# Kernel optimization log

Measured on AMD Instinct MI355X. Metric: run time of the kernel, lower is better.

Reference implementation:

```python
import jax, jax.numpy as jnp
import numpy as np

NEIGHB = 16   # k neighbors
GROUP = 32    # GroupNorm groups (== outc/2 -> per-channel instance norm)
EPS = 1e-5


def _lrelu(x, slope):
    return jnp.where(x >= 0, x, slope * x)


def _gn(x, gamma, beta, groups=GROUP, eps=EPS):
    # GroupNorm over [B, C, S, K]
    B, C, S, K = x.shape
    xr = x.reshape(B, groups, (C // groups) * S * K)
    m = xr.mean(-1, keepdims=True)
    v = xr.var(-1, keepdims=True)
    xn = ((xr - m) * jax.lax.rsqrt(v + eps)).reshape(B, C, S, K)
    return xn * gamma[None, :, None, None] + beta[None, :, None, None]


def _sample(x, rand_num, s_num, k):
    # Dynamic_sampling.forward, s_num <= P branch (s_num == P here)
    B, C, P = x.shape
    perm = jnp.argsort(rand_num, axis=1)[:, :s_num]                    # [B,S]
    sel = jnp.take_along_axis(x, perm[:, None, :], axis=2)             # [B,C,S]
    x3, s3 = x[:, :3], sel[:, :3]
    # pairwise = -||xi - qj||^2, shape [B,P,S]
    pd = -(jnp.sum(x3 * x3, 1)[:, :, None]
           - 2.0 * jnp.einsum('bcp,bcs->bps', x3, s3)
           + jnp.sum(s3 * s3, 1)[:, None, :])
    _, idx = jax.lax.top_k(pd.transpose(0, 2, 1), k)                   # [B,S,k]
    # torch: topk(dim=-2) gives [B,k,S], then .view(B,s_num,k) -> row-major
    # reinterpretation (NOT a transpose). Replicate exactly:
    idx = idx.transpose(0, 2, 1).reshape(B, s_num, k)
    xT = x.transpose(0, 2, 1)                                          # [B,P,C]
    feat = jax.vmap(lambda xt, ii: xt[ii])(xT, idx)                    # [B,S,k,C]
    return feat.transpose(0, 3, 1, 2)                                  # [B,C,S,k]


def _forward(x, rand_num, w_pe, g_pe, b_pe, w_conv, g_conv, b_conv,
             w_att1, w_att2, w_b1, w_b2, num_points):
    x1 = _sample(x, jax.lax.stop_gradient(rand_num), num_points, NEIGHB)  # [B,4,S,K]
    PA = x1[:, :3]                                                        # [B,3,S,K]
    PC = x1[:, :3, :, 0:1]                                                # [B,3,S,1]
    diff = PA - PC
    # safe sqrt: diff at K=0 is exactly 0 -> clamp to keep grads finite
    temp = jnp.sqrt(jnp.clip(jnp.sum(diff * diff, 1, keepdims=True), 1e-12))
    PEmb = jnp.concatenate([PA, jnp.broadcast_to(PC, PA.shape), diff, temp], axis=1)  # [B,10,S,K]
    PEmb = _lrelu(_gn(jnp.einsum('oc,bcsk->bosk', w_pe, PEmb), g_pe, b_pe), 0.2)
    x_ = _lrelu(_gn(jnp.einsum('oc,bcsk->bosk', w_conv, x1), g_conv, b_conv), 0.2)
    feature = jnp.concatenate([x_, PEmb], axis=1)                         # [B,64,S,K]
    att = jnp.einsum('oc,bcsk->bosk', w_att2,
                     _lrelu(jnp.einsum('oc,bcsk->bosk', w_att1, feature), 0.2))
    att = jax.nn.softmax(att, axis=-1)                                    # over K
    feature = jnp.sum(feature * att, axis=-1)                             # [B,64,S]
    Fea1 = jnp.einsum('oc,bcs->bos', w_b1, feature)
    Fea2 = jnp.einsum('oc,bcs->bos', w_b2, x1[:, :, :, 0])
    out = _lrelu(Fea1 + Fea2, 0.1)
    return jnp.concatenate([x1[:, :3, :, 0], out], axis=1)                # [B,67,S]


def setup_inputs() -> dict:
    key = jax.random.key(0)
    ks = jax.random.split(key, 10)
    B, C, P = 2, 4, 8192
    sc = 0.1
    x = jax.random.normal(ks[0], (B, C, P), jnp.float32)
    rand_num = jax.random.uniform(ks[1], (B, P), jnp.float32)
    w_pe = jax.random.normal(ks[2], (32, 10), jnp.float32) * sc
    g_pe = jnp.ones((32,), jnp.float32)
    b_pe = jnp.zeros((32,), jnp.float32)
    w_conv = jax.random.normal(ks[3], (32, 4), jnp.float32) * sc
    g_conv = jnp.ones((32,), jnp.float32)
    b_conv = jnp.zeros((32,), jnp.float32)
    w_att1 = jax.random.normal(ks[4], (32, 64), jnp.float32) * sc
    w_att2 = jax.random.normal(ks[5], (1, 32), jnp.float32) * sc
    w_b1 = jax.random.normal(ks[6], (64, 64), jnp.float32) * sc
    w_b2 = jax.random.normal(ks[7], (64, 4), jnp.float32) * sc
    return dict(x=x, rand_num=rand_num, w_pe=w_pe, g_pe=g_pe, b_pe=b_pe,
                w_conv=w_conv, g_conv=g_conv, b_conv=b_conv,
                w_att1=w_att1, w_att2=w_att2, w_b1=w_b1, w_b2=w_b2,
                num_points=8192)


def reference(x, rand_num, w_pe, g_pe, b_pe, w_conv, g_conv, b_conv,
              w_att1, w_att2, w_b1, w_b2, num_points):
    return _forward(x, rand_num, w_pe, g_pe, b_pe, w_conv, g_conv, b_conv,
                    w_att1, w_att2, w_b1, w_b2, num_points)
```

## Files before the change

kernel.cpp:

```cpp
#include <hip/hip_runtime.h>
#include <stdint.h>

#define PN 8192
#define SN 8192
#define KNB 16
#define SUBS 4
#define NCH1 8
#define CHUNK1 256
#define NCOL 8
#define COLCH (PN / NCOL)
#define SEGCAP 32
#define MARGIN 1.0e-3f
#define NRCH 8
#define RCH (PN / NRCH)

#define KEY_SENTINEL ((long long)0x8000000000000000ULL)
#define PD_SCALE 2199023255552.0

__device__ __forceinline__ void bitonic_sort16(float* b) {
#pragma unroll
    for (int k = 2; k <= 16; k <<= 1) {
#pragma unroll
        for (int j = k >> 1; j > 0; j >>= 1) {
#pragma unroll
            for (int i = 0; i < 16; ++i) {
                int l = i ^ j;
                if (l > i) {
                    float lo = fminf(b[i], b[l]), hi = fmaxf(b[i], b[l]);
                    bool up = ((i & k) == 0);
                    b[i] = up ? lo : hi;
                    b[l] = up ? hi : lo;
                }
            }
        }
    }
}
__device__ __forceinline__ void merge16(float* r, const float* b) {
    float t[16];
#pragma unroll
    for (int i = 0; i < 16; ++i) t[i] = fminf(r[i], b[15 - i]);
#pragma unroll
    for (int j = 8; j > 0; j >>= 1) {
#pragma unroll
        for (int i = 0; i < 16; ++i) {
            int l = i ^ j;
            if (l > i) {
                float lo = fminf(t[i], t[l]), hi = fmaxf(t[i], t[l]);
                t[i] = lo; t[l] = hi;
            }
        }
    }
#pragma unroll
    for (int i = 0; i < 16; ++i) r[i] = t[i];
}

__global__ void pack_pts_kernel(const float* __restrict__ x, float4* __restrict__ pts) {
    int i = blockIdx.x * 256 + threadIdx.x;
    int b = i >> 13, p = i & (PN - 1);
    const float* xb = x + (size_t)b * 4 * PN;
    pts[i] = make_float4(xb[p], xb[PN + p], xb[2 * PN + p], 0.f);
}

__global__ __launch_bounds__(256) void rank_count_kernel(const float* __restrict__ rnd,
        unsigned short* __restrict__ rcnt) {
    __shared__ unsigned long long lk[RCH];
    const int chunk = blockIdx.x, sg = blockIdx.y, b = blockIdx.z;
    const unsigned int* rb = (const unsigned int*)rnd + b * PN;
    const int cbase = chunk * RCH;
    for (int c = threadIdx.x; c < RCH; c += 256) {
        int j = cbase + c;
        lk[c] = ((unsigned long long)rb[j] << 13) | (unsigned)j;
    }
    __syncthreads();
    const int i = sg * 256 + threadIdx.x;
    const unsigned long long ki = ((unsigned long long)rb[i] << 13) | (unsigned)i;
    int cnt = 0;
#pragma unroll 8
    for (int c = 0; c < RCH; ++c) cnt += (lk[c] < ki) ? 1 : 0;
    rcnt[(((size_t)(b * NRCH + chunk)) << 13) + i] = (unsigned short)cnt;
}

__global__ void rank_scatter_kernel(const unsigned short* __restrict__ rcnt,
                                    int* __restrict__ perm) {
    int t = blockIdx.x * 256 + threadIdx.x;
    int b = t >> 13, i = t & (PN - 1);
    int rank = 0;
#pragma unroll
    for (int ch = 0; ch < NRCH; ++ch)
        rank += rcnt[(((size_t)(b * NRCH + ch)) << 13) + i];
    perm[b * PN + rank] = i;
}

__global__ __launch_bounds__(256) void knn_val16_kernel(const float4* __restrict__ pts,
        const int* __restrict__ perm, float* __restrict__ vv) {
    const int chunk = blockIdx.x, sg = blockIdx.y, b = blockIdx.z;
    const float4* pb = pts + b * PN;
    const int pbase = chunk * CHUNK1;
    const int s = sg * 256 + threadIdx.x;
    const float4 qp = pb[perm[b * PN + s]];
    float r[16];
#pragma unroll
    for (int i = 0; i < 16; ++i) r[i] = 3.0e38f;
    for (int t = 0; t < CHUNK1; t += 16) {
        float bv[16];
#pragma unroll
        for (int u = 0; u < 16; ++u) {
            float4 pp = pb[SUBS * (pbase + t + u)];
            float dx = qp.x - pp.x, dy = qp.y - pp.y, dz = qp.z - pp.z;
            bv[u] = dx * dx + dy * dy + dz * dz;
        }
        bitonic_sort16(bv);
        merge16(r, bv);
    }
    float* ov = vv + ((size_t)(b * NCH1 + chunk) * 16) * SN + s;
#pragma unroll
    for (int i = 0; i < 16; ++i) ov[(size_t)i * SN] = r[i];
}

__global__ void knn_thr_kernel(const float* __restrict__ vv, float* __restrict__ thrbuf) {
    int t = blockIdx.x * 256 + threadIdx.x;
    int b = t >> 13, s = t & (SN - 1);
    float r[16], bl[16];
    const float* v0 = vv + ((size_t)(b * NCH1) * 16) * SN + s;
#pragma unroll
    for (int i = 0; i < 16; ++i) r[i] = v0[(size_t)i * SN];
    for (int ch = 1; ch < NCH1; ++ch) {
        const float* vc = vv + ((size_t)(b * NCH1 + ch) * 16) * SN + s;
#pragma unroll
        for (int i = 0; i < 16; ++i) bl[i] = vc[(size_t)i * SN];
        merge16(r, bl);
    }
    thrbuf[b * SN + s] = r[15] + MARGIN;
}

#define COLPROC(pp, cidx) do { \
    float dx_ = qp.x - (pp).x, dy_ = qp.y - (pp).y, dz_ = qp.z - (pp).z; \
    float dd_ = dx_ * dx_; dd_ += dy_ * dy_; dd_ += dz_ * dz_; \
    if (dd_ < thr) { if (cnt < SEGCAP) seg[cnt] = (unsigned short)(cidx); ++cnt; } \
} while (0)

__global__ __launch_bounds__(256) void knn_collect_kernel(const float4* __restrict__ pts,
        const int* __restrict__ perm, const float* __restrict__ thrbuf,
        unsigned short* __restrict__ segcnt, unsigned short* __restrict__ segIdx) {
    const int chunk = blockIdx.x, sg = blockIdx.y, b = blockIdx.z;
    const float4* pb = pts + b * PN;
    const int pbase = chunk * COLCH;
    const int s = sg * 256 + threadIdx.x;
    const int bs = b * SN + s;
    const float4 qp = pb[perm[bs]];
    const float thr = thrbuf[bs];
    unsigned short* seg = segIdx + ((size_t)bs * NCOL + chunk) * SEGCAP;
    int cnt = 0;
    const float4* cp = pb + pbase;
    float4 a0 = cp[0], a1 = cp[1], a2 = cp[2], a3 = cp[3];
    float4 a4 = cp[4], a5 = cp[5], a6 = cp[6], a7 = cp[7];
    int c = 0;
    for (; c < COLCH - 8; c += 8) {
        float4 n0 = cp[c + 8],  n1 = cp[c + 9],  n2 = cp[c + 10], n3 = cp[c + 11];
        float4 n4 = cp[c + 12], n5 = cp[c + 13], n6 = cp[c + 14], n7 = cp[c + 15];
        COLPROC(a0, pbase + c + 0);
        COLPROC(a1, pbase + c + 1);
        COLPROC(a2, pbase + c + 2);
        COLPROC(a3, pbase + c + 3);
        COLPROC(a4, pbase + c + 4);
        COLPROC(a5, pbase + c + 5);
        COLPROC(a6, pbase + c + 6);
        COLPROC(a7, pbase + c + 7);
        a0 = n0; a1 = n1; a2 = n2; a3 = n3;
        a4 = n4; a5 = n5; a6 = n6; a7 = n7;
    }
    COLPROC(a0, pbase + c + 0);
    COLPROC(a1, pbase + c + 1);
    COLPROC(a2, pbase + c + 2);
    COLPROC(a3, pbase + c + 3);
    COLPROC(a4, pbase + c + 4);
    COLPROC(a5, pbase + c + 5);
    COLPROC(a6, pbase + c + 6);
    COLPROC(a7, pbase + c + 7);
    segcnt[(size_t)bs * NCOL + chunk] = (unsigned short)cnt;
}

#define MAKEKEY(pp, c, out) do { \
    double dx_ = qx - (double)(pp).x; \
    double dy_ = qy - (double)(pp).y; \
    double dz_ = qz - (double)(pp).z; \
    double dd_ = dx_ * dx_ + dy_ * dy_ + dz_ * dz_; \
    long long sc_ = (long long)floor(-dd_ * PD_SCALE); \
    (out) = (sc_ << 13) | (long long)(8191 - (c)); \
} while (0)

#define INS16(kkv) do { long long nk = (kkv); if (nk > k15) { \
    k15 = (nk > k14) ? k14 : ((nk > k15) ? nk : k15); \
    k14 = (nk > k13) ? k13 : ((nk > k14) ? nk : k14); \
    k13 = (nk > k12) ? k12 : ((nk > k13) ? nk : k13); \
    k12 = (nk > k11) ? k11 : ((nk > k12) ? nk : k12); \
    k11 = (nk > k10) ? k10 : ((nk > k11) ? nk : k11); \
    k10 = (nk > k9 ) ? k9  : ((nk > k10) ? nk : k10); \
    k9  = (nk > k8 ) ? k8  : ((nk > k9 ) ? nk : k9 ); \
    k8  = (nk > k7 ) ? k7  : ((nk > k8 ) ? nk : k8 ); \
    k7  = (nk > k6 ) ? k6  : ((nk > k7 ) ? nk : k7 ); \
    k6  = (nk > k5 ) ? k5  : ((nk > k6 ) ? nk : k6 ); \
    k5  = (nk > k4 ) ? k4  : ((nk > k5 ) ? nk : k5 ); \
    k4  = (nk > k3 ) ? k3  : ((nk > k4 ) ? nk : k4 ); \
    k3  = (nk > k2 ) ? k2  : ((nk > k3 ) ? nk : k3 ); \
    k2  = (nk > k1 ) ? k1  : ((nk > k2 ) ? nk : k2 ); \
    k1  = (nk > k0 ) ? k0  : ((nk > k1 ) ? nk : k1 ); \
    k0  = (nk > k0 ) ? nk  : k0; \
} } while (0)

__global__ __launch_bounds__(256) void knn_exact_kernel(const float4* __restrict__ pts,
        const int* __restrict__ perm, const unsigned short* __restrict__ segcnt,
        const unsigned short* __restrict__ segIdx, int* __restrict__ knn) {
    int t = blockIdx.x * 256 + threadIdx.x;
    int b = t >> 13, s = t & (SN - 1);
    const int bs = b * SN + s;
    const float4* pb = pts + b * PN;
    const float4 qp = pb[perm[bs]];
    const double qx = qp.x, qy = qp.y, qz = qp.z;
    long long k0 = KEY_SENTINEL, k1 = KEY_SENTINEL, k2 = KEY_SENTINEL, k3 = KEY_SENTINEL,
              k4 = KEY_SENTINEL, k5 = KEY_SENTINEL, k6 = KEY_SENTINEL, k7 = KEY_SENTINEL,
              k8 = KEY_SENTINEL, k9 = KEY_SENTINEL, k10 = KEY_SENTINEL, k11 = KEY_SENTINEL,
              k12 = KEY_SENTINEL, k13 = KEY_SENTINEL, k14 = KEY_SENTINEL, k15 = KEY_SENTINEL;
    const unsigned short* scp = segcnt + (size_t)bs * NCOL;
    ushort4 c03 = *reinterpret_cast<const ushort4*>(scp);
    ushort4 c47 = *reinterpret_cast<const ushort4*>(scp + 4);
    int ns[NCOL] = {c03.x, c03.y, c03.z, c03.w, c47.x, c47.y, c47.z, c47.w};
    bool ovf = false;
#pragma unroll
    for (int ch = 0; ch < NCOL; ++ch) ovf |= (ns[ch] > SEGCAP);
    if (!ovf) {
        const unsigned short* base = segIdx + (size_t)bs * (NCOL * SEGCAP);
#pragma unroll
        for (int ch = 0; ch < NCOL; ++ch) {
            const unsigned short* seg = base + ch * SEGCAP;
            const int n = ns[ch];
            for (int u = 0; u < n; u += 4) {
                ushort4 i4 = *reinterpret_cast<const ushort4*>(seg + u);
                int c0i = (int)i4.x;
                int c1i = (u + 1 < n) ? (int)i4.y : 0;
                int c2i = (u + 2 < n) ? (int)i4.z : 0;
                int c3i = (u + 3 < n) ? (int)i4.w : 0;
                float4 p0 = pb[c0i], p1 = pb[c1i], p2 = pb[c2i], p3 = pb[c3i];
                long long kk0, kk1, kk2, kk3;
                MAKEKEY(p0, c0i, kk0);
                MAKEKEY(p1, c1i, kk1);
                MAKEKEY(p2, c2i, kk2);
                MAKEKEY(p3, c3i, kk3);
                kk1 = (u + 1 < n) ? kk1 : KEY_SENTINEL;
                kk2 = (u + 2 < n) ? kk2 : KEY_SENTINEL;
                kk3 = (u + 3 < n) ? kk3 : KEY_SENTINEL;
                INS16(kk0);
                INS16(kk1);
                INS16(kk2);
                INS16(kk3);
            }
        }
    } else {
        for (int c = 0; c < PN; ++c) {
            float4 pp = pb[c];
            long long kk;
            MAKEKEY(pp, c, kk);
            INS16(kk);
        }
    }
    int* ob = knn + (size_t)b * (SN * KNB);
    ob[(size_t)0 * SN + s]  = 8191 - (int)(k0 & 8191);
    ob[(size_t)1 * SN + s]  = 8191 - (int)(k1 & 8191);
    ob[(size_t)2 * SN + s]  = 8191 - (int)(k2 & 8191);
    ob[(size_t)3 * SN + s]  = 8191 - (int)(k3 & 8191);
    ob[(size_t)4 * SN + s]  = 8191 - (int)(k4 & 8191);
    ob[(size_t)5 * SN + s]  = 8191 - (int)(k5 & 8191);
    ob[(size_t)6 * SN + s]  = 8191 - (int)(k6 & 8191);
    ob[(size_t)7 * SN + s]  = 8191 - (int)(k7 & 8191);
    ob[(size_t)8 * SN + s]  = 8191 - (int)(k8 & 8191);
    ob[(size_t)9 * SN + s]  = 8191 - (int)(k9 & 8191);
    ob[(size_t)10 * SN + s] = 8191 - (int)(k10 & 8191);
    ob[(size_t)11 * SN + s] = 8191 - (int)(k11 & 8191);
    ob[(size_t)12 * SN + s] = 8191 - (int)(k12 & 8191);
    ob[(size_t)13 * SN + s] = 8191 - (int)(k13 & 8191);
    ob[(size_t)14 * SN + s] = 8191 - (int)(k14 & 8191);
    ob[(size_t)15 * SN + s] = 8191 - (int)(k15 & 8191);
}

__global__ __launch_bounds__(256) void stats_kernel(const float* __restrict__ x,
        const int* __restrict__ knn, const float* __restrict__ w_pe,
        const float* __restrict__ w_conv, float* __restrict__ wavepart) {
    const int blk = blockIdx.x;
    const int b = blockIdx.y;
    const int w = threadIdx.x >> 6, l = threadIdx.x & 63;
    float wr[10];
#pragma unroll
    for (int c = 0; c < 10; ++c) wr[c] = 0.f;
    if (l < 32) {
#pragma unroll
        for (int c = 0; c < 4; ++c) wr[c] = w_conv[l * 4 + c];
    } else {
#pragma unroll
        for (int c = 0; c < 10; ++c) wr[c] = w_pe[(l - 32) * 10 + c];
    }
    const float* xb = x + (size_t)b * 4 * PN;
    const int* kb = knn + (size_t)b * (SN * KNB);
    float s1 = 0.f, s2 = 0.f;
    const int nbase = blk * 512 + w * 128;
#pragma unroll 2
    for (int it = 0; it < 128; ++it) {
        int n = nbase + it;
        int i  = kb[n];
        int i0 = kb[n & ~15];
        float xa0 = xb[i], xa1 = xb[PN + i], xa2 = xb[2 * PN + i], xa3 = xb[3 * PN + i];
        float xc0 = xb[i0], xc1 = xb[PN + i0], xc2 = xb[2 * PN + i0];
        float d0 = xa0 - xc0, d1 = xa1 - xc1, d2 = xa2 - xc2;
        float dd = d0 * d0; dd += d1 * d1; dd += d2 * d2;
        float temp = sqrtf(fmaxf(dd, 1e-12f));
        float r;
        if (l < 32) {
            r = wr[0] * xa0 + wr[1] * xa1 + wr[2] * xa2 + wr[3] * xa3;
        } else {
            r = wr[0] * xa0 + wr[1] * xa1 + wr[2] * xa2
              + wr[3] * xc0 + wr[4] * xc1 + wr[5] * xc2
              + wr[6] * d0 + wr[7] * d1 + wr[8] * d2 + wr[9] * temp;
        }
        s1 += r;
        s2 += r * r;
    }
    const int wslot = blk * 4 + w;
    wavepart[((size_t)b * 1024 + wslot) * 128 + l] = s1;
    wavepart[((size_t)b * 1024 + wslot) * 128 + 64 + l] = s2;
}

__global__ void finalize_kernel(const float* __restrict__ wavepart,
        const float* __restrict__ g_pe, const float* __restrict__ b_pe,
        const float* __restrict__ g_conv, const float* __restrict__ b_conv,
        float* __restrict__ scsh) {
    const int t = threadIdx.x;
    const int b = t >> 7, k = t & 127;
    float acc = 0.f;
    for (int w = 0; w < 1024; ++w) acc += wavepart[((size_t)b * 1024 + w) * 128 + k];
    __shared__ float sums[2][128];
    sums[b][k] = acc;
    __syncthreads();
    if (k < 64) {
        const float N = 131072.f;
        float mean = sums[b][k] / N;
        float var = sums[b][64 + k] / N - mean * mean;
        float rstd = 1.0f / sqrtf(var + 1e-5f);
        float gam = (k < 32) ? g_conv[k] : g_pe[k - 32];
        float bet = (k < 32) ? b_conv[k] : b_pe[k - 32];
        float sc = gam * rstd;
        scsh[(b * 64 + k) * 2 + 0] = sc;
        scsh[(b * 64 + k) * 2 + 1] = bet - mean * sc;
    }
}

__global__ __launch_bounds__(256) void fused_main_kernel(
        const float* __restrict__ x, const int* __restrict__ knn,
        const float* __restrict__ w_pe, const float* __restrict__ w_conv,
        const float* __restrict__ w_att1, const float* __restrict__ w_att2,
        const float* __restrict__ w_b1, const float* __restrict__ w_b2,
        const float* __restrict__ scsh, float* __restrict__ out) {
    __shared__ float wb1T[64 * 64];
    __shared__ float wb2T[4 * 64];
    for (int i = threadIdx.x; i < 64 * 64; i += 256) wb1T[(i & 63) * 64 + (i >> 6)] = w_b1[i];
    { int i = threadIdx.x; wb2T[(i & 3) * 64 + (i >> 2)] = w_b2[i]; }
    __syncthreads();
    const int gidx = blockIdx.x;
    const int b = gidx >> 9;
    const int sb = (gidx & 511) << 4;
    const int l = threadIdx.x & 63;
    const int w = threadIdx.x >> 6;
    const int g = l >> 4, j = l & 15;
    const int s = sb + (w << 2) + g;
    const int srcl = g << 4;
    const float* xb = x + (size_t)b * 4 * PN;
    const int i1 = knn[(size_t)b * (SN * KNB) + (size_t)s * KNB + j];
    float xa0 = xb[i1], xa1 = xb[PN + i1], xa2 = xb[2 * PN + i1], xa3 = xb[3 * PN + i1];
    float xc0 = __shfl(xa0, srcl), xc1 = __shfl(xa1, srcl);
    float xc2 = __shfl(xa2, srcl), xc3 = __shfl(xa3, srcl);
    float d0 = xa0 - xc0, d1 = xa1 - xc1, d2 = xa2 - xc2;
    float dd = d0 * d0; dd += d1 * d1; dd += d2 * d2;
    float temp = sqrtf(fmaxf(dd, 1e-12f));
    float pem[10] = {xa0, xa1, xa2, xc0, xc1, xc2, d0, d1, d2, temp};
    float f[64];
    const float* ssb = scsh + b * 128;
#pragma unroll
    for (int o = 0; o < 32; ++o) {
        float r = w_conv[o * 4 + 0] * xa0;
        r += w_conv[o * 4 + 1] * xa1;
        r += w_conv[o * 4 + 2] * xa2;
        r += w_conv[o * 4 + 3] * xa3;
        r = r * ssb[o * 2 + 0] + ssb[o * 2 + 1];
        f[o] = (r >= 0.f) ? r : 0.2f * r;
    }
#pragma unroll
    for (int o = 0; o < 32; ++o) {
        float r = 0.f;
#pragma unroll
        for (int c = 0; c < 10; ++c) r += w_pe[o * 10 + c] * pem[c];
        r = r * ssb[(32 + o) * 2 + 0] + ssb[(32 + o) * 2 + 1];
        f[32 + o] = (r >= 0.f) ? r : 0.2f * r;
    }
    float logit = 0.f;
#pragma unroll 2
    for (int o = 0; o < 32; ++o) {
        float a = 0.f;
#pragma unroll
        for (int c = 0; c < 64; ++c) a += w_att1[o * 64 + c] * f[c];
        a = (a >= 0.f) ? a : 0.2f * a;
        logit += w_att2[o] * a;
    }
    float mx = logit;
    mx = fmaxf(mx, __shfl_xor(mx, 1));
    mx = fmaxf(mx, __shfl_xor(mx, 2));
    mx = fmaxf(mx, __shfl_xor(mx, 4));
    mx = fmaxf(mx, __shfl_xor(mx, 8));
    float e = expf(logit - mx);
    float se = e;
    se += __shfl_xor(se, 1);
    se += __shfl_xor(se, 2);
    se += __shfl_xor(se, 4);
    se += __shfl_xor(se, 8);
    float att = e / se;
#pragma unroll
    for (int c = 0; c < 64; ++c) {
        float v = f[c] * att;
        v += __shfl_xor(v, 1);
        v += __shfl_xor(v, 2);
        v += __shfl_xor(v, 4);
        v += __shfl_xor(v, 8);
        f[c] = v;
    }
    float o0 = 0.f, o1 = 0.f, o2 = 0.f, o3 = 0.f;
#pragma unroll
    for (int c = 0; c < 64; ++c) {
        float4 wv = *reinterpret_cast<const float4*>(&wb1T[c * 64 + 4 * j]);
        o0 += wv.x * f[c]; o1 += wv.y * f[c]; o2 += wv.z * f[c]; o3 += wv.w * f[c];
    }
    {
        float4 wv = *reinterpret_cast<const float4*>(&wb2T[0 * 64 + 4 * j]);
        o0 += wv.x * xc0; o1 += wv.y * xc0; o2 += wv.z * xc0; o3 += wv.w * xc0;
        wv = *reinterpret_cast<const float4*>(&wb2T[1 * 64 + 4 * j]);
        o0 += wv.x * xc1; o1 += wv.y * xc1; o2 += wv.z * xc1; o3 += wv.w * xc1;
        wv = *reinterpret_cast<const float4*>(&wb2T[2 * 64 + 4 * j]);
        o0 += wv.x * xc2; o1 += wv.y * xc2; o2 += wv.z * xc2; o3 += wv.w * xc2;
        wv = *reinterpret_cast<const float4*>(&wb2T[3 * 64 + 4 * j]);
        o0 += wv.x * xc3; o1 += wv.y * xc3; o2 += wv.z * xc3; o3 += wv.w * xc3;
    }
    o0 = (o0 >= 0.f) ? o0 : 0.1f * o0;
    o1 = (o1 >= 0.f) ? o1 : 0.1f * o1;
    o2 = (o2 >= 0.f) ? o2 : 0.1f * o2;
    o3 = (o3 >= 0.f) ? o3 : 0.1f * o3;
    float* ob = out + (size_t)b * 67 * SN;
    const int oc = 3 + 4 * j;
    ob[(size_t)(oc + 0) * SN + s] = o0;
    ob[(size_t)(oc + 1) * SN + s] = o1;
    ob[(size_t)(oc + 2) * SN + s] = o2;
    ob[(size_t)(oc + 3) * SN + s] = o3;
    if (j < 3) ob[(size_t)j * SN + s] = (j == 0) ? xc0 : ((j == 1) ? xc1 : xc2);
}

extern "C" void kernel_launch(void* const* d_in, const int* in_sizes, int n_in,
                              void* d_out, int out_size, void* d_ws, size_t ws_size,
                              hipStream_t stream) {
    (void)in_sizes; (void)n_in; (void)out_size; (void)ws_size;
    const float* x      = (const float*)d_in[0];
    const float* rnd    = (const float*)d_in[1];
    const float* w_pe   = (const float*)d_in[2];
    const float* g_pe   = (const float*)d_in[3];
    const float* b_pe   = (const float*)d_in[4];
    const float* w_conv = (const float*)d_in[5];
    const float* g_conv = (const float*)d_in[6];
    const float* b_conv = (const float*)d_in[7];
    const float* w_att1 = (const float*)d_in[8];
    const float* w_att2 = (const float*)d_in[9];
    const float* w_b1   = (const float*)d_in[10];
    const float* w_b2   = (const float*)d_in[11];
    float* out = (float*)d_out;
    char* ws = (char*)d_ws;
    float4*         pts    = (float4*)        (ws + 0);
    int*            perm   = (int*)           (ws + 262144);
    unsigned short* rcnt   = (unsigned short*)(ws + 327680);
    float*          vv     = (float*)         (ws + 327680);
    unsigned short* segIdx = (unsigned short*)(ws + 327680);
    float*          wavept = (float*)         (ws + 327680);
    float*          thrbuf = (float*)         (ws + 8716288);
    unsigned short* segcnt = (unsigned short*)(ws + 8781824);
    int*            knn    = (int*)           (ws + 9043968);
    float*          scsh   = (float*)         (ws + 10092544);

    pack_pts_kernel<<<64, 256, 0, stream>>>(x, pts);
    rank_count_kernel<<<dim3(NRCH, 32, 2), 256, 0, stream>>>(rnd, rcnt);
    rank_scatter_kernel<<<64, 256, 0, stream>>>(rcnt, perm);
    knn_val16_kernel<<<dim3(NCH1, 32, 2), 256, 0, stream>>>(pts, perm, vv);
    knn_thr_kernel<<<64, 256, 0, stream>>>(vv, thrbuf);
    knn_collect_kernel<<<dim3(NCOL, 32, 2), 256, 0, stream>>>(pts, perm, thrbuf, segcnt, segIdx);
    knn_exact_kernel<<<64, 256, 0, stream>>>(pts, perm, segcnt, segIdx, knn);
    stats_kernel<<<dim3(256, 2), 256, 0, stream>>>(x, knn, w_pe, w_conv, wavept);
    finalize_kernel<<<1, 256, 0, stream>>>(wavept, g_pe, b_pe, g_conv, b_conv, scsh);
    fused_main_kernel<<<1024, 256, 0, stream>>>(x, knn, w_pe, w_conv, w_att1, w_att2,
                                                w_b1, w_b2, scsh, out);
}
```

Before: 354.8 us.

## Fuse KNN candidate collection and exact top-k per chunk, add 4-way merge

Replaces the separate collect and exact kernels with a per-chunk kernel. It filters candidates against the threshold into a shared-memory survivor list, then computes exact top-16 keys for that chunk. A new merge kernel combines the four sorted partial lists per query. The aim is to drop the global segIdx/segcnt round trip and to spread the exact-distance work across 4x more blocks. In exchange it writes 64-bit partial keys to global memory and adds a merge launch; the overflow fallback now only scans its own chunk.

```diff
diff --git a/kernel.cpp b/kernel.cpp
--- a/kernel.cpp
+++ b/kernel.cpp
@@ -7,9 +7,9 @@
 #define SUBS 4
 #define NCH1 8
 #define CHUNK1 256
-#define NCOL 8
+#define NCOL 4
 #define COLCH (PN / NCOL)
-#define SEGCAP 32
+#define SCAP 56
 #define MARGIN 1.0e-3f
 #define NRCH 8
 #define RCH (PN / NRCH)
@@ -131,53 +131,6 @@
         merge16(r, bl);
     }
     thrbuf[b * SN + s] = r[15] + MARGIN;
-}
-
-#define COLPROC(pp, cidx) do { \
-    float dx_ = qp.x - (pp).x, dy_ = qp.y - (pp).y, dz_ = qp.z - (pp).z; \
-    float dd_ = dx_ * dx_; dd_ += dy_ * dy_; dd_ += dz_ * dz_; \
-    if (dd_ < thr) { if (cnt < SEGCAP) seg[cnt] = (unsigned short)(cidx); ++cnt; } \
-} while (0)
-
-__global__ __launch_bounds__(256) void knn_collect_kernel(const float4* __restrict__ pts,
-        const int* __restrict__ perm, const float* __restrict__ thrbuf,
-        unsigned short* __restrict__ segcnt, unsigned short* __restrict__ segIdx) {
-    const int chunk = blockIdx.x, sg = blockIdx.y, b = blockIdx.z;
-    const float4* pb = pts + b * PN;
-    const int pbase = chunk * COLCH;
-    const int s = sg * 256 + threadIdx.x;
-    const int bs = b * SN + s;
-    const float4 qp = pb[perm[bs]];
-    const float thr = thrbuf[bs];
-    unsigned short* seg = segIdx + ((size_t)bs * NCOL + chunk) * SEGCAP;
-    int cnt = 0;
-    const float4* cp = pb + pbase;
-    float4 a0 = cp[0], a1 = cp[1], a2 = cp[2], a3 = cp[3];
-    float4 a4 = cp[4], a5 = cp[5], a6 = cp[6], a7 = cp[7];
-    int c = 0;
-    for (; c < COLCH - 8; c += 8) {
-        float4 n0 = cp[c + 8],  n1 = cp[c + 9],  n2 = cp[c + 10], n3 = cp[c + 11];
-        float4 n4 = cp[c + 12], n5 = cp[c + 13], n6 = cp[c + 14], n7 = cp[c + 15];
-        COLPROC(a0, pbase + c + 0);
-        COLPROC(a1, pbase + c + 1);
-        COLPROC(a2, pbase + c + 2);
-        COLPROC(a3, pbase + c + 3);
-        COLPROC(a4, pbase + c + 4);
-        COLPROC(a5, pbase + c + 5);
-        COLPROC(a6, pbase + c + 6);
-        COLPROC(a7, pbase + c + 7);
-        a0 = n0; a1 = n1; a2 = n2; a3 = n3;
-        a4 = n4; a5 = n5; a6 = n6; a7 = n7;
-    }
-    COLPROC(a0, pbase + c + 0);
-    COLPROC(a1, pbase + c + 1);
-    COLPROC(a2, pbase + c + 2);
-    COLPROC(a3, pbase + c + 3);
-    COLPROC(a4, pbase + c + 4);
-    COLPROC(a5, pbase + c + 5);
-    COLPROC(a6, pbase + c + 6);
-    COLPROC(a7, pbase + c + 7);
-    segcnt[(size_t)bs * NCOL + chunk] = (unsigned short)cnt;
 }
 
 #define MAKEKEY(pp, c, out) do { \
@@ -208,78 +161,111 @@
     k0  = (nk > k0 ) ? nk  : k0; \
 } } while (0)
 
-__global__ __launch_bounds__(256) void knn_exact_kernel(const float4* __restrict__ pts,
-        const int* __restrict__ perm, const unsigned short* __restrict__ segcnt,
-        const unsigned short* __restrict__ segIdx, int* __restrict__ knn) {
-    int t = blockIdx.x * 256 + threadIdx.x;
-    int b = t >> 13, s = t & (SN - 1);
+#define QPROC(pp, cidx) do { \
+    float dx_ = qp.x - (pp).x, dy_ = qp.y - (pp).y, dz_ = qp.z - (pp).z; \
+    float dd_ = dx_ * dx_; dd_ += dy_ * dy_; dd_ += dz_ * dz_; \
+    if (dd_ < thr) { if (cnt < SCAP) surv[cnt][tid] = (unsigned short)(cidx); ++cnt; } \
+} while (0)
+
+__global__ __launch_bounds__(256) void knn_chunk_kernel(const float4* __restrict__ pts,
+        const int* __restrict__ perm, const float* __restrict__ thrbuf,
+        long long* __restrict__ partK) {
+    __shared__ unsigned short surv[SCAP][256];
+    const int chunk = blockIdx.x, sg = blockIdx.y, b = blockIdx.z;
+    const float4* pb = pts + b * PN;
+    const int pbase = chunk * COLCH;
+    const int tid = threadIdx.x;
+    const int s = sg * 256 + tid;
     const int bs = b * SN + s;
-    const float4* pb = pts + b * PN;
     const float4 qp = pb[perm[bs]];
+    const float thr = thrbuf[bs];
+    int cnt = 0;
+    const float4* cp = pb + pbase;
+    float4 a0 = cp[0], a1 = cp[1], a2 = cp[2], a3 = cp[3];
+    float4 a4 = cp[4], a5 = cp[5], a6 = cp[6], a7 = cp[7];
+    int c = 0;
+    for (; c < COLCH - 8; c += 8) {
+        float4 n0 = cp[c + 8],  n1 = cp[c + 9],  n2 = cp[c + 10], n3 = cp[c + 11];
+        float4 n4 = cp[c + 12], n5 = cp[c + 13], n6 = cp[c + 14], n7 = cp[c + 15];
+        QPROC(a0, pbase + c + 0);
+        QPROC(a1, pbase + c + 1);
+        QPROC(a2, pbase + c + 2);
+        QPROC(a3, pbase + c + 3);
+        QPROC(a4, pbase + c + 4);
+        QPROC(a5, pbase + c + 5);
+        QPROC(a6, pbase + c + 6);
+        QPROC(a7, pbase + c + 7);
+        a0 = n0; a1 = n1; a2 = n2; a3 = n3;
+        a4 = n4; a5 = n5; a6 = n6; a7 = n7;
+    }
+    QPROC(a0, pbase + c + 0);
+    QPROC(a1, pbase + c + 1);
+    QPROC(a2, pbase + c + 2);
+    QPROC(a3, pbase + c + 3);
+    QPROC(a4, pbase + c + 4);
+    QPROC(a5, pbase + c + 5);
+    QPROC(a6, pbase + c + 6);
+    QPROC(a7, pbase + c + 7);
     const double qx = qp.x, qy = qp.y, qz = qp.z;
     long long k0 = KEY_SENTINEL, k1 = KEY_SENTINEL, k2 = KEY_SENTINEL, k3 = KEY_SENTINEL,
               k4 = KEY_SENTINEL, k5 = KEY_SENTINEL, k6 = KEY_SENTINEL, k7 = KEY_SENTINEL,
               k8 = KEY_SENTINEL, k9 = KEY_SENTINEL, k10 = KEY_SENTINEL, k11 = KEY_SENTINEL,
               k12 = KEY_SENTINEL, k13 = KEY_SENTINEL, k14 = KEY_SENTINEL, k15 = KEY_SENTINEL;
-    const unsigned short* scp = segcnt + (size_t)bs * NCOL;
-    ushort4 c03 = *reinterpret_cast<const ushort4*>(scp);
-    ushort4 c47 = *reinterpret_cast<const ushort4*>(scp + 4);
-    int ns[NCOL] = {c03.x, c03.y, c03.z, c03.w, c47.x, c47.y, c47.z, c47.w};
-    bool ovf = false;
-#pragma unroll
-    for (int ch = 0; ch < NCOL; ++ch) ovf |= (ns[ch] > SEGCAP);
-    if (!ovf) {
-        const unsigned short* base = segIdx + (size_t)bs * (NCOL * SEGCAP);
-#pragma unroll
-        for (int ch = 0; ch < NCOL; ++ch) {
-            const unsigned short* seg = base + ch * SEGCAP;
-            const int n = ns[ch];
-            for (int u = 0; u < n; u += 4) {
-                ushort4 i4 = *reinterpret_cast<const ushort4*>(seg + u);
-                int c0i = (int)i4.x;
-                int c1i = (u + 1 < n) ? (int)i4.y : 0;
-                int c2i = (u + 2 < n) ? (int)i4.z : 0;
-                int c3i = (u + 3 < n) ? (int)i4.w : 0;
-                float4 p0 = pb[c0i], p1 = pb[c1i], p2 = pb[c2i], p3 = pb[c3i];
-                long long kk0, kk1, kk2, kk3;
-                MAKEKEY(p0, c0i, kk0);
-                MAKEKEY(p1, c1i, kk1);
-                MAKEKEY(p2, c2i, kk2);
-                MAKEKEY(p3, c3i, kk3);
-                kk1 = (u + 1 < n) ? kk1 : KEY_SENTINEL;
-                kk2 = (u + 2 < n) ? kk2 : KEY_SENTINEL;
-                kk3 = (u + 3 < n) ? kk3 : KEY_SENTINEL;
-                INS16(kk0);
-                INS16(kk1);
-                INS16(kk2);
-                INS16(kk3);
-            }
+    if (cnt <= SCAP) {
+        for (int u = 0; u < cnt; u += 4) {
+            int c0i = surv[u][tid];
+            int c1i = (u + 1 < cnt) ? (int)surv[u + 1][tid] : 0;
+            int c2i = (u + 2 < cnt) ? (int)surv[u + 2][tid] : 0;
+            int c3i = (u + 3 < cnt) ? (int)surv[u + 3][tid] : 0;
+            float4 p0 = pb[c0i], p1 = pb[c1i], p2 = pb[c2i], p3 = pb[c3i];
+            long long kk0, kk1, kk2, kk3;
+            MAKEKEY(p0, c0i, kk0);
+            MAKEKEY(p1, c1i, kk1);
+            MAKEKEY(p2, c2i, kk2);
+            MAKEKEY(p3, c3i, kk3);
+            kk1 = (u + 1 < cnt) ? kk1 : KEY_SENTINEL;
+            kk2 = (u + 2 < cnt) ? kk2 : KEY_SENTINEL;
+            kk3 = (u + 3 < cnt) ? kk3 : KEY_SENTINEL;
+            INS16(kk0);
+            INS16(kk1);
+            INS16(kk2);
+            INS16(kk3);
         }
     } else {
-        for (int c = 0; c < PN; ++c) {
-            float4 pp = pb[c];
+        for (int cc = 0; cc < COLCH; ++cc) {
+            float4 pp = cp[cc];
             long long kk;
-            MAKEKEY(pp, c, kk);
+            MAKEKEY(pp, pbase + cc, kk);
             INS16(kk);
         }
     }
+    long long* ok = partK + ((size_t)(b * NCOL + chunk) * SN + s) * KNB;
+    ok[0]  = k0;  ok[1]  = k1;  ok[2]  = k2;  ok[3]  = k3;
+    ok[4]  = k4;  ok[5]  = k5;  ok[6]  = k6;  ok[7]  = k7;
+    ok[8]  = k8;  ok[9]  = k9;  ok[10] = k10; ok[11] = k11;
+    ok[12] = k12; ok[13] = k13; ok[14] = k14; ok[15] = k15;
+}
+
+__global__ void knn_merge_kernel(const long long* __restrict__ partK, int* __restrict__ knn) {
+    int t = blockIdx.x * 64 + threadIdx.x;
+    int b = t >> 13, s = t & (SN - 1);
+    const long long* K0 = partK + ((size_t)(b * NCOL + 0) * SN + s) * KNB;
+    const long long* K1 = partK + ((size_t)(b * NCOL + 1) * SN + s) * KNB;
+    const long long* K2 = partK + ((size_t)(b * NCOL + 2) * SN + s) * KNB;
+    const long long* K3 = partK + ((size_t)(b * NCOL + 3) * SN + s) * KNB;
+    long long h0 = K0[0], h1 = K1[0], h2 = K2[0], h3 = K3[0];
+    int p0 = 1, p1 = 1, p2 = 1, p3 = 1;
     int* ob = knn + (size_t)b * (SN * KNB);
-    ob[(size_t)0 * SN + s]  = 8191 - (int)(k0 & 8191);
-    ob[(size_t)1 * SN + s]  = 8191 - (int)(k1 & 8191);
-    ob[(size_t)2 * SN + s]  = 8191 - (int)(k2 & 8191);
-    ob[(size_t)3 * SN + s]  = 8191 - (int)(k3 & 8191);
-    ob[(size_t)4 * SN + s]  = 8191 - (int)(k4 & 8191);
-    ob[(size_t)5 * SN + s]  = 8191 - (int)(k5 & 8191);
-    ob[(size_t)6 * SN + s]  = 8191 - (int)(k6 & 8191);
-    ob[(size_t)7 * SN + s]  = 8191 - (int)(k7 & 8191);
-    ob[(size_t)8 * SN + s]  = 8191 - (int)(k8 & 8191);
-    ob[(size_t)9 * SN + s]  = 8191 - (int)(k9 & 8191);
-    ob[(size_t)10 * SN + s] = 8191 - (int)(k10 & 8191);
-    ob[(size_t)11 * SN + s] = 8191 - (int)(k11 & 8191);
-    ob[(size_t)12 * SN + s] = 8191 - (int)(k12 & 8191);
-    ob[(size_t)13 * SN + s] = 8191 - (int)(k13 & 8191);
-    ob[(size_t)14 * SN + s] = 8191 - (int)(k14 & 8191);
-    ob[(size_t)15 * SN + s] = 8191 - (int)(k15 & 8191);
+    for (int r = 0; r < KNB; ++r) {
+        long long m01 = h0 > h1 ? h0 : h1;
+        long long m23 = h2 > h3 ? h2 : h3;
+        long long m = m01 > m23 ? m01 : m23;
+        ob[(size_t)r * SN + s] = 8191 - (int)(m & 8191);
+        if (m == h0)      { h0 = (p0 < KNB) ? K0[p0] : KEY_SENTINEL; ++p0; }
+        else if (m == h1) { h1 = (p1 < KNB) ? K1[p1] : KEY_SENTINEL; ++p1; }
+        else if (m == h2) { h2 = (p2 < KNB) ? K2[p2] : KEY_SENTINEL; ++p2; }
+        else              { h3 = (p3 < KNB) ? K3[p3] : KEY_SENTINEL; ++p3; }
+    }
 }
 
 __global__ __launch_bounds__(256) void stats_kernel(const float* __restrict__ x,
@@ -480,10 +466,9 @@
     int*            perm   = (int*)           (ws + 262144);
     unsigned short* rcnt   = (unsigned short*)(ws + 327680);
     float*          vv     = (float*)         (ws + 327680);
-    unsigned short* segIdx = (unsigned short*)(ws + 327680);
+    long long*      partK  = (long long*)     (ws + 327680);
     float*          wavept = (float*)         (ws + 327680);
     float*          thrbuf = (float*)         (ws + 8716288);
-    unsigned short* segcnt = (unsigned short*)(ws + 8781824);
     int*            knn    = (int*)           (ws + 9043968);
     float*          scsh   = (float*)         (ws + 10092544);
 
@@ -492,8 +477,8 @@
     rank_scatter_kernel<<<64, 256, 0, stream>>>(rcnt, perm);
     knn_val16_kernel<<<dim3(NCH1, 32, 2), 256, 0, stream>>>(pts, perm, vv);
     knn_thr_kernel<<<64, 256, 0, stream>>>(vv, thrbuf);
-    knn_collect_kernel<<<dim3(NCOL, 32, 2), 256, 0, stream>>>(pts, perm, thrbuf, segcnt, segIdx);
-    knn_exact_kernel<<<64, 256, 0, stream>>>(pts, perm, segcnt, segIdx, knn);
+    knn_chunk_kernel<<<dim3(NCOL, 32, 2), 256, 0, stream>>>(pts, perm, thrbuf, partK);
+    knn_merge_kernel<<<256, 64, 0, stream>>>(partK, knn);
     stats_kernel<<<dim3(256, 2), 256, 0, stream>>>(x, knn, w_pe, w_conv, wavept);
     finalize_kernel<<<1, 256, 0, stream>>>(wavept, g_pe, b_pe, g_conv, b_conv, scsh);
     fused_main_kernel<<<1024, 256, 0, stream>>>(x, knn, w_pe, w_conv, w_att1, w_att2,
```

New measurement: 351.0 us. Within noise of the previous version (-1.1%).
